# Optimization experiments

Measured on AMD Instinct MI355X. Metric: run time of the kernel, lower is better.

## Reference

```python
import jax, jax.numpy as jnp
import numpy as np

EMBED_DIM = 128

def setup_inputs() -> dict:
    key = jax.random.key(0)
    k_x, k_wf, k_bf, k_wo, k_bo = jax.random.split(key, 5)
    C = EMBED_DIM
    x = jax.random.normal(k_x, (4, 4096, C), dtype=jnp.float32)
    # Linear(C, 3C): weight applied as x @ W_fc + b_fc with W_fc [C, 3C]
    W_fc = jax.random.normal(k_wf, (C, 3 * C), dtype=jnp.float32) * (1.0 / np.sqrt(C))
    b_fc = jax.random.normal(k_bf, (3 * C,), dtype=jnp.float32) * 0.01
    W_out = jax.random.normal(k_wo, (C, C), dtype=jnp.float32) * (1.0 / np.sqrt(C))
    b_out = jax.random.normal(k_bo, (C,), dtype=jnp.float32) * 0.01
    scale = jnp.ones((1,), dtype=jnp.float32)
    return {"x": x, "W_fc": W_fc, "b_fc": b_fc, "W_out": W_out, "b_out": b_out, "scale": scale}

def reference(x, W_fc, b_fc, W_out, b_out, scale):
    C = x.shape[-1]
    qkv = x @ W_fc + b_fc                      # [B, N, 3C]
    q, k, v = jnp.split(qkv, 3, axis=-1)       # each [B, N, C]
    # scores: [B, N, N], scaled by 1/sqrt(C) then by learnable 1/scale
    attn = jnp.einsum('bnc,bmc->bnm', q, k) / jnp.sqrt(jnp.float32(C))
    attn = jax.nn.softmax(attn / scale[0], axis=-1)
    out = jnp.einsum('bnm,bmc->bnc', attn, v)   # [B, N, C]
    return out @ W_out + b_out
```

## Files before the change

kernel.cpp:

```cpp
#include <hip/hip_runtime.h>
#include <math.h>


typedef __attribute__((ext_vector_type(8))) short bf16x8;
typedef __attribute__((ext_vector_type(4))) short bf16x4;
typedef __attribute__((ext_vector_type(4))) float f32x4;
typedef __attribute__((ext_vector_type(2))) unsigned int u32x2;

#define M2EXP 17.3124f

static __device__ __forceinline__ short f2bf(float f) {
    union { float f; unsigned int u; } c; c.f = f;
    unsigned int u = c.u;
    unsigned int r = (u + 0x7FFFu + ((u >> 16) & 1u)) >> 16;
    return (short)(r & 0xFFFFu);
}
static __device__ __forceinline__ float bf2f(short v) {
    union { unsigned int u; float f; } c;
    c.u = ((unsigned int)(unsigned short)v) << 16;
    return c.f;
}
static __device__ __forceinline__ unsigned int cvt_pk_bf16(float lo, float hi) {
    unsigned int r;
    asm("v_cvt_pk_bf16_f32 %0, %1, %2" : "=v"(r) : "v"(lo), "v"(hi));
    return r;
}

__global__ __launch_bounds__(256) void transpose_w(const float* __restrict__ Wfc,
                                                   const float* __restrict__ Wout,
                                                   short* __restrict__ WfcT,
                                                   short* __restrict__ WoT) {
    __shared__ short T[64][72];
    const int bid = blockIdx.x;
    const float* src; short* dst; int S, n0, k0;
    if (bid < 12) { src = Wfc; dst = WfcT; S = 384; n0 = (bid % 6) * 64; k0 = (bid / 6) * 64; }
    else { int b2 = bid - 12; src = Wout; dst = WoT; S = 128; n0 = (b2 % 2) * 64; k0 = (b2 / 2) * 64; }
    const int t = threadIdx.x;
    {
        int kk = t >> 4, nn = (t & 15) * 4;
        for (int it = 0; it < 4; ++it) {
            int k = kk + it * 16;
            float4 f = *(const float4*)&src[(k0 + k) * S + n0 + nn];
            short4 s;
            s.x = f2bf(f.x); s.y = f2bf(f.y); s.z = f2bf(f.z); s.w = f2bf(f.w);
            *(short4*)&T[k][nn] = s;
        }
    }
    __syncthreads();
    {
        int nl = t >> 2, kg = (t & 3) * 16;
        bf16x8 v0, v1;
        for (int j = 0; j < 8; ++j) { v0[j] = T[kg + j][nl]; v1[j] = T[kg + 8 + j][nl]; }
        *(bf16x8*)&dst[(n0 + nl) * 128 + k0 + kg] = v0;
        *(bf16x8*)&dst[(n0 + nl) * 128 + k0 + kg + 8] = v1;
    }
}

__global__ __launch_bounds__(256) void qkv_kernel(
    const float* __restrict__ x, const short* __restrict__ WfcT,
    const float* __restrict__ bfc, const float* __restrict__ scale,
    short* __restrict__ Qs, short* __restrict__ Kb, short* __restrict__ VT) {
    __shared__ short Xs[32][136];
    __shared__ short Vs[128][40];
    const int t = threadIdx.x;
    const int rb = blockIdx.x;
    const int lane = t & 63, w = t >> 6;
    const int m16 = lane & 15, quad = lane >> 4;
    {
        int row = t >> 3, cg = t & 7;
        const float* src = &x[(rb * 32 + row) * 128 + cg * 16];
        float4 f0 = *(const float4*)&src[0];
        float4 f1 = *(const float4*)&src[4];
        float4 f2 = *(const float4*)&src[8];
        float4 f3 = *(const float4*)&src[12];
        bf16x8 v0, v1;
        v0[0] = f2bf(f0.x); v0[1] = f2bf(f0.y); v0[2] = f2bf(f0.z); v0[3] = f2bf(f0.w);
        v0[4] = f2bf(f1.x); v0[5] = f2bf(f1.y); v0[6] = f2bf(f1.z); v0[7] = f2bf(f1.w);
        v1[0] = f2bf(f2.x); v1[1] = f2bf(f2.y); v1[2] = f2bf(f2.z); v1[3] = f2bf(f2.w);
        v1[4] = f2bf(f3.x); v1[5] = f2bf(f3.y); v1[6] = f2bf(f3.z); v1[7] = f2bf(f3.w);
        *(bf16x8*)&Xs[row][cg * 16] = v0;
        *(bf16x8*)&Xs[row][cg * 16 + 8] = v1;
    }
    __syncthreads();

    bf16x8 a[2][4];
    for (int rt = 0; rt < 2; ++rt)
        for (int kc = 0; kc < 4; ++kc)
            a[rt][kc] = *(const bf16x8*)&Xs[rt * 16 + m16][kc * 32 + quad * 8];

    const float sfac = 1.44269504088896f / (sqrtf(128.0f) * scale[0]);

#pragma unroll
    for (int i = 0; i < 6; ++i) {
        const int gct = w * 6 + i;
        bf16x8 bfr[4];
        for (int kc = 0; kc < 4; ++kc)
            bfr[kc] = *(const bf16x8*)&WfcT[(gct * 16 + m16) * 128 + kc * 32 + quad * 8];
        f32x4 acc[2];
        for (int rt = 0; rt < 2; ++rt)
            for (int j = 0; j < 4; ++j) acc[rt][j] = 0.0f;
        for (int kc = 0; kc < 4; ++kc) {
            acc[0] = __builtin_amdgcn_mfma_f32_16x16x32_bf16(a[0][kc], bfr[kc], acc[0], 0, 0, 0);
            acc[1] = __builtin_amdgcn_mfma_f32_16x16x32_bf16(a[1][kc], bfr[kc], acc[1], 0, 0, 0);
        }
        const int c = gct * 16 + m16;
        const float bias = bfc[c];
        if (gct < 8) {
            for (int rt = 0; rt < 2; ++rt)
                for (int r = 0; r < 4; ++r)
                    Qs[(rb * 32 + rt * 16 + quad * 4 + r) * 128 + c] =
                        f2bf((acc[rt][r] + bias) * sfac);
        } else if (gct < 16) {
            for (int rt = 0; rt < 2; ++rt)
                for (int r = 0; r < 4; ++r)
                    Kb[(rb * 32 + rt * 16 + quad * 4 + r) * 128 + (c - 128)] =
                        f2bf(acc[rt][r] + bias);
        } else {
            const int ch = c - 256;
            for (int rt = 0; rt < 2; ++rt)
                for (int r = 0; r < 4; ++r)
                    Vs[ch][rt * 16 + quad * 4 + r] = f2bf(acc[rt][r] + bias);
        }
    }
    __syncthreads();
    {
        int ch = t >> 1, seg = t & 1;
        int b_ = (rb * 32) >> 12, nn = (rb * 32) & 4095;
        uint4 u0 = *(const uint4*)&Vs[ch][seg * 16];
        uint4 u1 = *(const uint4*)&Vs[ch][seg * 16 + 8];
        short* dstp = &VT[((size_t)b_ * 128 + ch) * 4096 + nn + seg * 16];
        *(uint4*)&dstp[0] = u0;
        *(uint4*)&dstp[8] = u1;
    }
}

__global__ __launch_bounds__(256, 2) void flash_kernel(
    const short* __restrict__ Qs, const short* __restrict__ Kb,
    const short* __restrict__ VT, short* __restrict__ Opart,
    float* __restrict__ Lpart, int nsplit) {
    __shared__ short Kst[2 * 64 * 128];
    __shared__ short VTs[2 * 128 * 64];
    __shared__ short Ps[128 * 64];

    const int t = threadIdx.x;
    const int lane = t & 63, w = t >> 6;
    const int m16 = lane & 15, quad = lane >> 4;
    const int kvq = blockIdx.x >> 7;
    const int bqt = blockIdx.x & 127;
    const int batch = bqt & 3;
    const int qt = bqt >> 2;
    const int iters = 64 / nsplit;
    const int qlen = 4096 / nsplit;

    bf16x8 qf[2][4];
    for (int rh = 0; rh < 2; ++rh) {
        const short* qb = Qs + (batch * 4096 + qt * 128 + w * 32 + rh * 16 + m16) * 128;
        for (int kc = 0; kc < 4; ++kc)
            qf[rh][kc] = *(const bf16x8*)&qb[kc * 32 + quad * 8];
    }

    f32x4 acc_o[2][8];
    for (int rh = 0; rh < 2; ++rh)
        for (int i = 0; i < 8; ++i)
            for (int j = 0; j < 4; ++j) acc_o[rh][i][j] = 0.0f;
    float lsum[2] = {0.f, 0.f};

    const short* kbase = Kb + (batch * 4096 + kvq * qlen) * 128;
    const short* vbase = VT + (batch * 128) * 4096 + kvq * qlen;

    const int krl = lane >> 4, kslot = lane & 15;
    const int vrl = lane >> 3, vslot = lane & 7;
    const int qs7 = m16 & 7;

#define STAGE_KV(TILE, BUF)                                                       \
    {                                                                             \
        const int koff_ = (BUF) * (64 * 128);                                     \
        const int voff_ = (BUF) * (128 * 64);                                     \
        for (int j = 0; j < 4; ++j) {                                             \
            int krow = w * 16 + j * 4 + krl;                                      \
            int gch = kslot ^ (krow & 15);                                        \
            __builtin_amdgcn_global_load_lds(                                     \
                (const __attribute__((address_space(1))) void*)                   \
                    &kbase[((TILE) * 64 + krow) * 128 + gch * 8],                 \
                (__attribute__((address_space(3))) void*)                         \
                    &Kst[koff_ + (w * 16 + j * 4) * 128],                         \
                16, 0, 0);                                                        \
        }                                                                         \
        for (int j = 0; j < 4; ++j) {                                             \
            int vrow = w * 32 + j * 8 + vrl;                                      \
            int gch = vslot ^ (vrow & 7);                                         \
            __builtin_amdgcn_global_load_lds(                                     \
                (const __attribute__((address_space(1))) void*)                   \
                    &vbase[vrow * 4096 + (TILE) * 64 + gch * 8],                  \
                (__attribute__((address_space(3))) void*)                         \
                    &VTs[voff_ + (w * 32 + j * 8) * 64],                          \
                16, 0, 0);                                                        \
        }                                                                         \
    }

#define COMPUTE_TILE(BUF)                                                         \
    {                                                                             \
        const int koff_ = (BUF) * (64 * 128);                                     \
        const int voff_ = (BUF) * (128 * 64);                                     \
        f32x4 s[2][4];                                                            \
        for (int rh = 0; rh < 2; ++rh)                                            \
            for (int i = 0; i < 4; ++i)                                           \
                for (int j = 0; j < 4; ++j) s[rh][i][j] = 0.0f;                   \
        __builtin_amdgcn_s_setprio(1);                                            \
        for (int kc = 0; kc < 4; ++kc) {                                          \
            for (int ct = 0; ct < 4; ++ct) {                                      \
                bf16x8 ak = *(const bf16x8*)&Kst[koff_ + (ct * 16 + m16) * 128 +  \
                                                 (((4 * kc + quad) ^ m16) << 3)]; \
                s[0][ct] = __builtin_amdgcn_mfma_f32_16x16x32_bf16(               \
                    ak, qf[0][kc], s[0][ct], 0, 0, 0);                            \
                s[1][ct] = __builtin_amdgcn_mfma_f32_16x16x32_bf16(               \
                    ak, qf[1][kc], s[1][ct], 0, 0, 0);                            \
            }                                                                     \
        }                                                                         \
        __builtin_amdgcn_s_setprio(0);                                            \
        for (int rh = 0; rh < 2; ++rh) {                                          \
            const int q_ = w * 32 + rh * 16 + m16;                                \
            for (int ct = 0; ct < 4; ++ct) {                                      \
                float p0 = __builtin_amdgcn_exp2f(s[rh][ct][0] - M2EXP);          \
                float p1 = __builtin_amdgcn_exp2f(s[rh][ct][1] - M2EXP);          \
                float p2 = __builtin_amdgcn_exp2f(s[rh][ct][2] - M2EXP);          \
                float p3 = __builtin_amdgcn_exp2f(s[rh][ct][3] - M2EXP);          \
                lsum[rh] += (p0 + p1) + (p2 + p3);                                \
                u32x2 pw;                                                         \
                pw[0] = cvt_pk_bf16(p0, p1);                                      \
                pw[1] = cvt_pk_bf16(p2, p3);                                      \
                const int c16_ = ct * 2 + (quad >> 1);                            \
                *(u32x2*)&Ps[q_ * 64 + ((c16_ ^ qs7) << 3) + ((quad & 1) << 2)] = \
                    pw;                                                           \
            }                                                                     \
        }                                                                         \
        __builtin_amdgcn_s_setprio(1);                                            \
        for (int kc2 = 0; kc2 < 2; ++kc2) {                                       \
            bf16x8 a2[2];                                                         \
            for (int rh = 0; rh < 2; ++rh) {                                      \
                const int q_ = w * 32 + rh * 16 + m16;                            \
                a2[rh] = *(const bf16x8*)&Ps[q_ * 64 +                            \
                                             (((kc2 * 4 + quad) ^ qs7) << 3)];    \
            }                                                                     \
            for (int ot = 0; ot < 8; ++ot) {                                      \
                int vr_ = ot * 16 + m16;                                          \
                bf16x8 b2 = *(const bf16x8*)&VTs[voff_ + vr_ * 64 +               \
                                                 (((4 * kc2 + quad) ^ (vr_ & 7)) << 3)]; \
                acc_o[0][ot] = __builtin_amdgcn_mfma_f32_16x16x32_bf16(           \
                    a2[0], b2, acc_o[0][ot], 0, 0, 0);                            \
                acc_o[1][ot] = __builtin_amdgcn_mfma_f32_16x16x32_bf16(           \
                    a2[1], b2, acc_o[1][ot], 0, 0, 0);                            \
            }                                                                     \
        }                                                                         \
        __builtin_amdgcn_s_setprio(0);                                            \
    }

    STAGE_KV(0, 0);

    for (int kt = 0; kt < iters; kt += 2) {
        __syncthreads();
        STAGE_KV(kt + 1, 1);
        COMPUTE_TILE(0);
        __syncthreads();
        if (kt + 2 < iters) STAGE_KV(kt + 2, 0);
        COMPUTE_TILE(1);
    }

    for (int rh = 0; rh < 2; ++rh) {
        lsum[rh] += __shfl_xor(lsum[rh], 16, 64);
        lsum[rh] += __shfl_xor(lsum[rh], 32, 64);
    }

    __syncthreads();
    short* Ot = Kst;
    for (int rh = 0; rh < 2; ++rh)
        for (int ot = 0; ot < 8; ++ot)
            for (int r = 0; r < 4; ++r) {
                int row = w * 32 + rh * 16 + quad * 4 + r;
                int col = ot * 16 + m16;
                Ot[row * 128 + ((((col >> 3) ^ (row & 15)) << 3)) + (col & 7)] =
                    f2bf(acc_o[rh][ot][r]);
            }
    if (quad == 0) {
        for (int rh = 0; rh < 2; ++rh) {
            const int rowb = batch * 4096 + qt * 128 + w * 32 + rh * 16 + m16;
            Lpart[kvq * 16384 + rowb] = lsum[rh];
        }
    }
    __syncthreads();
    {
        short* obase = Opart + (size_t)kvq * 16384 * 128 +
                       (size_t)(batch * 4096 + qt * 128) * 128;
        int c = t & 15;
        for (int p = 0; p < 8; ++p) {
            int row = p * 16 + (t >> 4);
            uint4 v = *(const uint4*)&Ot[row * 128 + ((c ^ (row & 15)) << 3)];
            *(uint4*)&obase[row * 128 + c * 8] = v;
        }
    }
#undef STAGE_KV
#undef COMPUTE_TILE
}

__global__ __launch_bounds__(256) void mergeproj_kernel(
    const short* __restrict__ Opart, const float* __restrict__ Lpart,
    const short* __restrict__ WoT, const float* __restrict__ bout,
    float* __restrict__ out, int nsplit) {
    __shared__ short Os[16][136];
    const int t = threadIdx.x;
    const int rb = blockIdx.x;
    const int lane = t & 63, w = t >> 6;
    const int m16 = lane & 15, quad = lane >> 4;
    {
        int row = rb * 16 + (t >> 4), col = (t & 15) * 8;
        float a[8] = {0, 0, 0, 0, 0, 0, 0, 0};
        float lt = 0;
        for (int q = 0; q < nsplit; ++q) {
            bf16x8 v8 = *(const bf16x8*)&Opart[((size_t)q * 16384 + row) * 128 + col];
            for (int j = 0; j < 8; ++j) a[j] += bf2f(v8[j]);
            lt += Lpart[q * 16384 + row];
        }
        float rl = 1.0f / lt;
        bf16x8 v;
        for (int j = 0; j < 8; ++j) v[j] = f2bf(a[j] * rl);
        *(bf16x8*)&Os[t >> 4][col] = v;
    }
    __syncthreads();
    f32x4 acc[2];
    for (int i = 0; i < 2; ++i)
        for (int j = 0; j < 4; ++j) acc[i][j] = 0.0f;
    for (int kc = 0; kc < 4; ++kc) {
        bf16x8 a = *(const bf16x8*)&Os[m16][kc * 32 + quad * 8];
        for (int c2 = 0; c2 < 2; ++c2) {
            int ct = w * 2 + c2;
            bf16x8 b = *(const bf16x8*)&WoT[(ct * 16 + m16) * 128 + kc * 32 + quad * 8];
            acc[c2] = __builtin_amdgcn_mfma_f32_16x16x32_bf16(a, b, acc[c2], 0, 0, 0);
        }
    }
    for (int c2 = 0; c2 < 2; ++c2) {
        int ct = w * 2 + c2;
        int c = ct * 16 + m16;
        float bias = bout[c];
        for (int r = 0; r < 4; ++r)
            out[(rb * 16 + quad * 4 + r) * 128 + c] = acc[c2][r] + bias;
    }
}

extern "C" void kernel_launch(void* const* d_in, const int* in_sizes, int n_in,
                              void* d_out, int out_size, void* d_ws, size_t ws_size,
                              hipStream_t stream) {
    const float* x     = (const float*)d_in[0];
    const float* Wfc   = (const float*)d_in[1];
    const float* bfc   = (const float*)d_in[2];
    const float* Wout  = (const float*)d_in[3];
    const float* bout  = (const float*)d_in[4];
    const float* scale = (const float*)d_in[5];
    float* out = (float*)d_out;

    char* ws = (char*)d_ws;
    short* WfcT = (short*)(ws);
    short* WoT  = (short*)(ws + 98304);
    short* Qs   = (short*)(ws + 131072);
    short* Kb   = (short*)(ws + 131072 + 4194304);
    short* VT   = (short*)(ws + 131072 + 2 * 4194304);
    const size_t base = 131072 + (size_t)3 * 4194304;
    short* Opart = (short*)(ws + base);
    const size_t opart1 = (size_t)16384 * 128 * 2;
    const size_t lpart1 = (size_t)16384 * 4;
    int nsplit;
    if (ws_size >= base + 4 * opart1 + 4 * lpart1) nsplit = 4;
    else if (ws_size >= base + 2 * opart1 + 2 * lpart1) nsplit = 2;
    else nsplit = 1;
    float* Lpart = (float*)(ws + base + (size_t)nsplit * opart1);

    hipLaunchKernelGGL(transpose_w, dim3(16), dim3(256), 0, stream, Wfc, Wout, WfcT, WoT);
    hipLaunchKernelGGL(qkv_kernel, dim3(512), dim3(256), 0, stream, x, WfcT, bfc, scale, Qs, Kb, VT);
    hipLaunchKernelGGL(flash_kernel, dim3(128 * nsplit), dim3(256), 0, stream,
                       Qs, Kb, VT, Opart, Lpart, nsplit);
    hipLaunchKernelGGL(mergeproj_kernel, dim3(1024), dim3(256), 0, stream,
                       Opart, Lpart, WoT, bout, out, nsplit);
}
```

Baseline: 126.2 us.

## Fuse weight transpose into QKV and merge/projection into flash via atomic flags

The weight transpose moves into the QKV kernel as its first 16 blocks, which raise a global counter that the other blocks spin on. The merge and output-projection work moves into the flash kernel: the last of the two KV-split blocks for each query tile merges the partials and applies W_out. The KV split is fixed at 2, and QKV blocks now process 64 rows each. This removes two kernel launches and the inter-kernel gaps, at the cost of a memset, spin-waits that assume all blocks are co-resident, and a serialized tail on the last-arriving block.

```diff
diff --git a/kernel.cpp b/kernel.cpp
--- a/kernel.cpp
+++ b/kernel.cpp
@@ -3,7 +3,6 @@
 
 
 typedef __attribute__((ext_vector_type(8))) short bf16x8;
-typedef __attribute__((ext_vector_type(4))) short bf16x4;
 typedef __attribute__((ext_vector_type(4))) float f32x4;
 typedef __attribute__((ext_vector_type(2))) unsigned int u32x2;
 
@@ -26,65 +25,75 @@
     return r;
 }
 
-__global__ __launch_bounds__(256) void transpose_w(const float* __restrict__ Wfc,
-                                                   const float* __restrict__ Wout,
-                                                   short* __restrict__ WfcT,
-                                                   short* __restrict__ WoT) {
-    __shared__ short T[64][72];
+__global__ __launch_bounds__(256) void qkv_kernel(
+    const float* __restrict__ x, const float* __restrict__ Wfc,
+    const float* __restrict__ bfc, const float* __restrict__ Wout,
+    const float* __restrict__ scale,
+    short* __restrict__ WfcT, short* __restrict__ WoT,
+    short* __restrict__ Qs, short* __restrict__ Kb, short* __restrict__ VT,
+    int* wflag) {
+    __shared__ __align__(16) char smem[35840];
+    const int t = threadIdx.x;
     const int bid = blockIdx.x;
-    const float* src; short* dst; int S, n0, k0;
-    if (bid < 12) { src = Wfc; dst = WfcT; S = 384; n0 = (bid % 6) * 64; k0 = (bid / 6) * 64; }
-    else { int b2 = bid - 12; src = Wout; dst = WoT; S = 128; n0 = (b2 % 2) * 64; k0 = (b2 / 2) * 64; }
-    const int t = threadIdx.x;
-    {
-        int kk = t >> 4, nn = (t & 15) * 4;
-        for (int it = 0; it < 4; ++it) {
-            int k = kk + it * 16;
-            float4 f = *(const float4*)&src[(k0 + k) * S + n0 + nn];
-            short4 s;
-            s.x = f2bf(f.x); s.y = f2bf(f.y); s.z = f2bf(f.z); s.w = f2bf(f.w);
-            *(short4*)&T[k][nn] = s;
-        }
-    }
-    __syncthreads();
-    {
-        int nl = t >> 2, kg = (t & 3) * 16;
-        bf16x8 v0, v1;
-        for (int j = 0; j < 8; ++j) { v0[j] = T[kg + j][nl]; v1[j] = T[kg + 8 + j][nl]; }
-        *(bf16x8*)&dst[(n0 + nl) * 128 + k0 + kg] = v0;
-        *(bf16x8*)&dst[(n0 + nl) * 128 + k0 + kg + 8] = v1;
-    }
-}
-
-__global__ __launch_bounds__(256) void qkv_kernel(
-    const float* __restrict__ x, const short* __restrict__ WfcT,
-    const float* __restrict__ bfc, const float* __restrict__ scale,
-    short* __restrict__ Qs, short* __restrict__ Kb, short* __restrict__ VT) {
-    __shared__ short Xs[32][136];
-    __shared__ short Vs[128][40];
-    const int t = threadIdx.x;
-    const int rb = blockIdx.x;
     const int lane = t & 63, w = t >> 6;
     const int m16 = lane & 15, quad = lane >> 4;
+
+    if (bid < 16) {
+        short (*T)[72] = (short(*)[72])smem;
+        const float* src; short* dst; int S, n0, k0;
+        if (bid < 12) { src = Wfc; dst = WfcT; S = 384; n0 = (bid % 6) * 64; k0 = (bid / 6) * 64; }
+        else { int b2 = bid - 12; src = Wout; dst = WoT; S = 128; n0 = (b2 & 1) * 64; k0 = (b2 >> 1) * 64; }
+        {
+            int kk = t >> 4, nn = (t & 15) * 4;
+            for (int it = 0; it < 4; ++it) {
+                int k = kk + it * 16;
+                float4 f = *(const float4*)&src[(k0 + k) * S + n0 + nn];
+                short4 s4;
+                s4.x = f2bf(f.x); s4.y = f2bf(f.y); s4.z = f2bf(f.z); s4.w = f2bf(f.w);
+                *(short4*)&T[k][nn] = s4;
+            }
+        }
+        __syncthreads();
+        {
+            int nl = t >> 2, kg = (t & 3) * 16;
+            bf16x8 v0, v1;
+            for (int j = 0; j < 8; ++j) { v0[j] = T[kg + j][nl]; v1[j] = T[kg + 8 + j][nl]; }
+            *(bf16x8*)&dst[(n0 + nl) * 128 + k0 + kg] = v0;
+            *(bf16x8*)&dst[(n0 + nl) * 128 + k0 + kg + 8] = v1;
+        }
+        __syncthreads();
+        if (t == 0) {
+            __builtin_amdgcn_fence(__ATOMIC_RELEASE, "agent");
+            atomicAdd(wflag, 1);
+        }
+        return;
+    }
+
+    const int rb = bid - 16;
+    short (*Xs)[136] = (short(*)[136])smem;
+    short (*Vs)[72]  = (short(*)[72])(smem + 17408);
     {
-        int row = t >> 3, cg = t & 7;
-        const float* src = &x[(rb * 32 + row) * 128 + cg * 16];
-        float4 f0 = *(const float4*)&src[0];
-        float4 f1 = *(const float4*)&src[4];
-        float4 f2 = *(const float4*)&src[8];
-        float4 f3 = *(const float4*)&src[12];
-        bf16x8 v0, v1;
-        v0[0] = f2bf(f0.x); v0[1] = f2bf(f0.y); v0[2] = f2bf(f0.z); v0[3] = f2bf(f0.w);
-        v0[4] = f2bf(f1.x); v0[5] = f2bf(f1.y); v0[6] = f2bf(f1.z); v0[7] = f2bf(f1.w);
-        v1[0] = f2bf(f2.x); v1[1] = f2bf(f2.y); v1[2] = f2bf(f2.z); v1[3] = f2bf(f2.w);
-        v1[4] = f2bf(f3.x); v1[5] = f2bf(f3.y); v1[6] = f2bf(f3.z); v1[7] = f2bf(f3.w);
-        *(bf16x8*)&Xs[row][cg * 16] = v0;
-        *(bf16x8*)&Xs[row][cg * 16 + 8] = v1;
-    }
-    __syncthreads();
-
-    bf16x8 a[2][4];
-    for (int rt = 0; rt < 2; ++rt)
+        int row = t >> 2, cg4 = (t & 3) * 32;
+        const float* src = &x[(rb * 64 + row) * 128 + cg4];
+        for (int h = 0; h < 4; ++h) {
+            float4 f0 = *(const float4*)&src[h * 8];
+            float4 f1 = *(const float4*)&src[h * 8 + 4];
+            bf16x8 v;
+            v[0] = f2bf(f0.x); v[1] = f2bf(f0.y); v[2] = f2bf(f0.z); v[3] = f2bf(f0.w);
+            v[4] = f2bf(f1.x); v[5] = f2bf(f1.y); v[6] = f2bf(f1.z); v[7] = f2bf(f1.w);
+            *(bf16x8*)&Xs[row][cg4 + h * 8] = v;
+        }
+    }
+    __syncthreads();
+    if (t == 0) {
+        while (__atomic_load_n(wflag, __ATOMIC_ACQUIRE) < 16)
+            __builtin_amdgcn_s_sleep(2);
+    }
+    __syncthreads();
+    __builtin_amdgcn_fence(__ATOMIC_ACQUIRE, "agent");
+
+    bf16x8 a[4][4];
+    for (int rt = 0; rt < 4; ++rt)
         for (int kc = 0; kc < 4; ++kc)
             a[rt][kc] = *(const bf16x8*)&Xs[rt * 16 + m16][kc * 32 + quad * 8];
 
@@ -96,61 +105,65 @@
         bf16x8 bfr[4];
         for (int kc = 0; kc < 4; ++kc)
             bfr[kc] = *(const bf16x8*)&WfcT[(gct * 16 + m16) * 128 + kc * 32 + quad * 8];
-        f32x4 acc[2];
-        for (int rt = 0; rt < 2; ++rt)
+        f32x4 acc[4];
+        for (int rt = 0; rt < 4; ++rt)
             for (int j = 0; j < 4; ++j) acc[rt][j] = 0.0f;
-        for (int kc = 0; kc < 4; ++kc) {
-            acc[0] = __builtin_amdgcn_mfma_f32_16x16x32_bf16(a[0][kc], bfr[kc], acc[0], 0, 0, 0);
-            acc[1] = __builtin_amdgcn_mfma_f32_16x16x32_bf16(a[1][kc], bfr[kc], acc[1], 0, 0, 0);
-        }
+        for (int kc = 0; kc < 4; ++kc)
+            for (int rt = 0; rt < 4; ++rt)
+                acc[rt] = __builtin_amdgcn_mfma_f32_16x16x32_bf16(a[rt][kc], bfr[kc], acc[rt], 0, 0, 0);
         const int c = gct * 16 + m16;
         const float bias = bfc[c];
         if (gct < 8) {
-            for (int rt = 0; rt < 2; ++rt)
+            for (int rt = 0; rt < 4; ++rt)
                 for (int r = 0; r < 4; ++r)
-                    Qs[(rb * 32 + rt * 16 + quad * 4 + r) * 128 + c] =
+                    Qs[(rb * 64 + rt * 16 + quad * 4 + r) * 128 + c] =
                         f2bf((acc[rt][r] + bias) * sfac);
         } else if (gct < 16) {
-            for (int rt = 0; rt < 2; ++rt)
+            for (int rt = 0; rt < 4; ++rt)
                 for (int r = 0; r < 4; ++r)
-                    Kb[(rb * 32 + rt * 16 + quad * 4 + r) * 128 + (c - 128)] =
+                    Kb[(rb * 64 + rt * 16 + quad * 4 + r) * 128 + (c - 128)] =
                         f2bf(acc[rt][r] + bias);
         } else {
             const int ch = c - 256;
-            for (int rt = 0; rt < 2; ++rt)
+            for (int rt = 0; rt < 4; ++rt)
                 for (int r = 0; r < 4; ++r)
                     Vs[ch][rt * 16 + quad * 4 + r] = f2bf(acc[rt][r] + bias);
         }
     }
     __syncthreads();
     {
-        int ch = t >> 1, seg = t & 1;
-        int b_ = (rb * 32) >> 12, nn = (rb * 32) & 4095;
-        uint4 u0 = *(const uint4*)&Vs[ch][seg * 16];
-        uint4 u1 = *(const uint4*)&Vs[ch][seg * 16 + 8];
-        short* dstp = &VT[((size_t)b_ * 128 + ch) * 4096 + nn + seg * 16];
-        *(uint4*)&dstp[0] = u0;
-        *(uint4*)&dstp[8] = u1;
+        int ch = t >> 1, half = (t & 1) * 32;
+        int b_ = (rb * 64) >> 12, nn = (rb * 64) & 4095;
+        short* dstp = &VT[((size_t)(b_ * 128 + ch)) * 4096 + nn + half];
+        const short* sp = &Vs[ch][half];
+        *(uint4*)&dstp[0]  = *(const uint4*)&sp[0];
+        *(uint4*)&dstp[8]  = *(const uint4*)&sp[8];
+        *(uint4*)&dstp[16] = *(const uint4*)&sp[16];
+        *(uint4*)&dstp[24] = *(const uint4*)&sp[24];
     }
 }
 
 __global__ __launch_bounds__(256, 2) void flash_kernel(
     const short* __restrict__ Qs, const short* __restrict__ Kb,
-    const short* __restrict__ VT, short* __restrict__ Opart,
-    float* __restrict__ Lpart, int nsplit) {
-    __shared__ short Kst[2 * 64 * 128];
-    __shared__ short VTs[2 * 128 * 64];
-    __shared__ short Ps[128 * 64];
+    const short* __restrict__ VT, const short* __restrict__ WoT,
+    const float* __restrict__ bout,
+    short* __restrict__ Opart, float* __restrict__ Lpart,
+    int* mflag, float* __restrict__ out) {
+    __shared__ __align__(16) char smem[81920];
+    short* Kst = (short*)smem;
+    short* VTs = (short*)(smem + 32768);
+    short* Ps  = (short*)(smem + 65536);
 
     const int t = threadIdx.x;
+    const int bid = blockIdx.x;
     const int lane = t & 63, w = t >> 6;
     const int m16 = lane & 15, quad = lane >> 4;
-    const int kvq = blockIdx.x >> 7;
-    const int bqt = blockIdx.x & 127;
+    const int kvq = bid >> 7;
+    const int bqt = bid & 127;
     const int batch = bqt & 3;
     const int qt = bqt >> 2;
-    const int iters = 64 / nsplit;
-    const int qlen = 4096 / nsplit;
+    const int iters = 32;
+    const int qlen = 2048;
 
     bf16x8 qf[2][4];
     for (int rh = 0; rh < 2; ++rh) {
@@ -256,7 +269,6 @@
     }
 
     STAGE_KV(0, 0);
-
     for (int kt = 0; kt < iters; kt += 2) {
         __syncthreads();
         STAGE_KV(kt + 1, 1);
@@ -265,6 +277,8 @@
         if (kt + 2 < iters) STAGE_KV(kt + 2, 0);
         COMPUTE_TILE(1);
     }
+#undef STAGE_KV
+#undef COMPUTE_TILE
 
     for (int rh = 0; rh < 2; ++rh) {
         lsum[rh] += __shfl_xor(lsum[rh], 16, 64);
@@ -298,51 +312,54 @@
             *(uint4*)&obase[row * 128 + c * 8] = v;
         }
     }
-#undef STAGE_KV
-#undef COMPUTE_TILE
-}
-
-__global__ __launch_bounds__(256) void mergeproj_kernel(
-    const short* __restrict__ Opart, const float* __restrict__ Lpart,
-    const short* __restrict__ WoT, const float* __restrict__ bout,
-    float* __restrict__ out, int nsplit) {
-    __shared__ short Os[16][136];
-    const int t = threadIdx.x;
-    const int rb = blockIdx.x;
-    const int lane = t & 63, w = t >> 6;
-    const int m16 = lane & 15, quad = lane >> 4;
-    {
-        int row = rb * 16 + (t >> 4), col = (t & 15) * 8;
-        float a[8] = {0, 0, 0, 0, 0, 0, 0, 0};
-        float lt = 0;
-        for (int q = 0; q < nsplit; ++q) {
-            bf16x8 v8 = *(const bf16x8*)&Opart[((size_t)q * 16384 + row) * 128 + col];
-            for (int j = 0; j < 8; ++j) a[j] += bf2f(v8[j]);
-            lt += Lpart[q * 16384 + row];
-        }
-        float rl = 1.0f / lt;
-        bf16x8 v;
-        for (int j = 0; j < 8; ++j) v[j] = f2bf(a[j] * rl);
-        *(bf16x8*)&Os[t >> 4][col] = v;
-    }
-    __syncthreads();
-    f32x4 acc[2];
-    for (int i = 0; i < 2; ++i)
-        for (int j = 0; j < 4; ++j) acc[i][j] = 0.0f;
-    for (int kc = 0; kc < 4; ++kc) {
-        bf16x8 a = *(const bf16x8*)&Os[m16][kc * 32 + quad * 8];
-        for (int c2 = 0; c2 < 2; ++c2) {
-            int ct = w * 2 + c2;
-            bf16x8 b = *(const bf16x8*)&WoT[(ct * 16 + m16) * 128 + kc * 32 + quad * 8];
-            acc[c2] = __builtin_amdgcn_mfma_f32_16x16x32_bf16(a, b, acc[c2], 0, 0, 0);
-        }
-    }
-    for (int c2 = 0; c2 < 2; ++c2) {
-        int ct = w * 2 + c2;
-        int c = ct * 16 + m16;
-        float bias = bout[c];
-        for (int r = 0; r < 4; ++r)
-            out[(rb * 16 + quad * 4 + r) * 128 + c] = acc[c2][r] + bias;
+
+    __syncthreads();
+    volatile int* sflag = (volatile int*)(smem + 81920 - 16);
+    if (t == 0) {
+        __builtin_amdgcn_fence(__ATOMIC_RELEASE, "agent");
+        *sflag = atomicAdd(&mflag[bqt], 1);
+    }
+    __syncthreads();
+    if (*sflag == 1) {
+        __builtin_amdgcn_fence(__ATOMIC_ACQUIRE, "agent");
+        short (*Os)[136] = (short(*)[136])smem;
+        {
+            int row = t >> 1, ch0 = (t & 1) * 64;
+            size_t gr = (size_t)batch * 4096 + qt * 128 + row;
+            float lt = Lpart[gr] + Lpart[16384 + gr];
+            float rl = 1.0f / lt;
+            for (int h = 0; h < 8; ++h) {
+                bf16x8 v0 = *(const bf16x8*)&Opart[gr * 128 + ch0 + h * 8];
+                bf16x8 v1 = *(const bf16x8*)&Opart[((size_t)16384 * 128) * 1 +
+                                                   gr * 128 + ch0 + h * 8 +
+                                                   (size_t)0];
+                bf16x8 o;
+                for (int j = 0; j < 8; ++j)
+                    o[j] = f2bf((bf2f(v0[j]) + bf2f(v1[j])) * rl);
+                *(bf16x8*)&Os[row][ch0 + h * 8] = o;
+            }
+        }
+        __syncthreads();
+        for (int e = 0; e < 2; ++e) {
+            const int rt = w * 2 + e;
+            bf16x8 a[4];
+            for (int kc = 0; kc < 4; ++kc)
+                a[kc] = *(const bf16x8*)&Os[rt * 16 + m16][kc * 32 + quad * 8];
+#pragma unroll
+            for (int ct = 0; ct < 8; ++ct) {
+                f32x4 acc;
+                for (int j = 0; j < 4; ++j) acc[j] = 0.0f;
+                for (int kc = 0; kc < 4; ++kc) {
+                    bf16x8 b = *(const bf16x8*)&WoT[(ct * 16 + m16) * 128 + kc * 32 + quad * 8];
+                    acc = __builtin_amdgcn_mfma_f32_16x16x32_bf16(a[kc], b, acc, 0, 0, 0);
+                }
+                const int c = ct * 16 + m16;
+                const float bias = bout[c];
+                for (int r = 0; r < 4; ++r)
+                    out[((size_t)batch * 4096 + qt * 128 + rt * 16 + quad * 4 + r) * 128 + c] =
+                        acc[r] + bias;
+            }
+        }
     }
 }
 
@@ -366,17 +383,14 @@
     const size_t base = 131072 + (size_t)3 * 4194304;
     short* Opart = (short*)(ws + base);
     const size_t opart1 = (size_t)16384 * 128 * 2;
-    const size_t lpart1 = (size_t)16384 * 4;
-    int nsplit;
-    if (ws_size >= base + 4 * opart1 + 4 * lpart1) nsplit = 4;
-    else if (ws_size >= base + 2 * opart1 + 2 * lpart1) nsplit = 2;
-    else nsplit = 1;
-    float* Lpart = (float*)(ws + base + (size_t)nsplit * opart1);
-
-    hipLaunchKernelGGL(transpose_w, dim3(16), dim3(256), 0, stream, Wfc, Wout, WfcT, WoT);
-    hipLaunchKernelGGL(qkv_kernel, dim3(512), dim3(256), 0, stream, x, WfcT, bfc, scale, Qs, Kb, VT);
-    hipLaunchKernelGGL(flash_kernel, dim3(128 * nsplit), dim3(256), 0, stream,
-                       Qs, Kb, VT, Opart, Lpart, nsplit);
-    hipLaunchKernelGGL(mergeproj_kernel, dim3(1024), dim3(256), 0, stream,
-                       Opart, Lpart, WoT, bout, out, nsplit);
-}
+    float* Lpart = (float*)(ws + base + 2 * opart1);
+    char* flags  = ws + base + 2 * opart1 + 131072;
+    int* wflag = (int*)flags;
+    int* mflag = (int*)(flags + 64);
+
+    hipMemsetAsync(flags, 0, 1024, stream);
+    hipLaunchKernelGGL(qkv_kernel, dim3(272), dim3(256), 0, stream,
+                       x, Wfc, bfc, Wout, scale, WfcT, WoT, Qs, Kb, VT, wflag);
+    hipLaunchKernelGGL(flash_kernel, dim3(256), dim3(256), 0, stream,
+                       Qs, Kb, VT, WoT, bout, Opart, Lpart, mflag, out);
+}
```

Result: slower. 166.9 us (+32.3%).
